# Kernel optimization log

Hardware: AMD Instinct MI355X
Metric: run time of the kernel (lower is better)

The kernel has to match this reference:

```python
import jax, jax.numpy as jnp
import numpy as np

B, L, D, K, NFFT = 4, 8192, 768, 24, 16384


def setup_inputs() -> dict:
    key = jax.random.key(0)
    k1, k2, k3, k4 = jax.random.split(key, 4)
    x = jax.random.normal(k1, (B, L, D), dtype=jnp.float32)
    phi = jax.random.normal(k2, (L, K), dtype=jnp.float32) * 0.1
    M_inputs = jax.random.normal(k3, (D, D), dtype=jnp.float32) * 0.02
    M_filters = jax.random.normal(k4, (K, D), dtype=jnp.float32) * 0.02
    return {"x": x, "phi": phi, "M_inputs": M_inputs, "M_filters": M_filters, "n": NFFT}


def _convolve_approx(u, v, n):
    # u: (B, L, D) projected inputs; v: (L, D) projected filters (per-channel kernels)
    bsz, seq_len, d = u.shape
    sgn = jnp.where(jnp.arange(seq_len) % 2 == 0, 1.0, -1.0).astype(u.dtype)[None, :, None]  # (1,L,1)
    V = jnp.fft.rfft(v.astype(jnp.float32), n=n, axis=0)[None, :, :, None]  # (1,F,D,1)
    U = jnp.stack([u, u * sgn], axis=-1).astype(jnp.float32)  # (B,L,D,2): [plus, sign-flipped]
    Uf = jnp.fft.rfft(U, n=n, axis=1)  # (B,F,D,2)
    conv = jnp.fft.irfft(V * Uf, n=n, axis=1)[:, :seq_len]  # (B,L,D,2)
    U_plus = conv[..., 0]
    U_minus = conv[..., 1] * sgn
    return U_plus, U_minus


def reference(x, phi, M_inputs, M_filters, n):
    x_proj = x @ M_inputs          # (B,L,D)
    phi_proj = phi @ M_filters     # (L,D)
    spectral_plus, spectral_minus = _convolve_approx(x_proj, phi_proj, n)
    return spectral_plus + spectral_minus
```

## Files before the change

### kernel.cpp

```cpp
#include <hip/hip_runtime.h>
#include <stdint.h>

#define B_SZ 4
#define L_SEQ 8192
#define D_CH 768
#define K_F 24
#define NFFT2 8192
#define LDS_BYTES 69632
#define GEMM_LDS 49152

typedef __attribute__((ext_vector_type(4))) float f32x4;
typedef __attribute__((ext_vector_type(8))) __bf16 bf16x8;
typedef __attribute__((ext_vector_type(2))) float v2f;

__device__ __forceinline__ uint32_t f2bf1(float f) {
  uint32_t u = __float_as_uint(f);
  return (u + 0x7fffu + ((u >> 16) & 1u)) >> 16;
}
__device__ __forceinline__ uint32_t packbf2(float lo, float hi) {
  return f2bf1(lo) | (f2bf1(hi) << 16);
}
__device__ __forceinline__ v2f unpackbf2(uint32_t v) {
  return v2f{__uint_as_float(v << 16), __uint_as_float(v & 0xffff0000u)};
}
__device__ __forceinline__ uint32_t pkbf(float lo, float hi) {
  uint32_t r;
  asm("v_cvt_pk_bf16_f32 %0, %1, %2" : "=v"(r) : "v"(lo), "v"(hi));
  return r;
}

__device__ __forceinline__ v2f rotm(v2f v) { return v2f{v.y, -v.x}; }
__device__ __forceinline__ v2f rotp(v2f v) { return v2f{-v.y, v.x}; }
__device__ __forceinline__ v2f cmulf(v2f a, v2f b) {
  return a.x * b + a.y * rotp(b);
}

__device__ __forceinline__ void twfill(v2f* tw) {
  tw[1] = cmulf(tw[0], tw[0]);
  tw[3] = cmulf(tw[1], tw[1]);
  tw[2] = cmulf(tw[0], tw[1]);
  tw[4] = cmulf(tw[3], tw[0]);
  tw[5] = cmulf(tw[3], tw[1]);
  tw[6] = cmulf(tw[3], tw[2]);
}

__global__ __launch_bounds__(256) void k_mit(const float* __restrict__ Mi,
                                             uint16_t* __restrict__ MiT) {
  int i = blockIdx.x * 256 + threadIdx.x;
  int n = i / 768, e = i - n * 768;
  MiT[i] = (uint16_t)f2bf1(Mi[e * 768 + n]);
}

template <int S>
__device__ __forceinline__ void dft8(v2f* x) {
  const float C = 0.70710678118654752f;
  v2f t0 = x[0] + x[4], t1 = x[0] - x[4];
  v2f t2 = x[2] + x[6], t3 = x[2] - x[6];
  v2f t4 = x[1] + x[5], t5 = x[1] - x[5];
  v2f t6 = x[3] + x[7], t7 = x[3] - x[7];
  v2f t3r = (S < 0) ? rotm(t3) : rotp(t3);
  v2f t7r = (S < 0) ? rotm(t7) : rotp(t7);
  v2f e0 = t0 + t2, e2 = t0 - t2;
  v2f e1 = t1 + t3r, e3 = t1 - t3r;
  v2f o0 = t4 + t6, o2 = t4 - t6;
  v2f o1 = t5 + t7r, o3 = t5 - t7r;
  v2f o1r = (S < 0) ? C * (o1 + rotm(o1)) : C * (o1 + rotp(o1));
  v2f o2r = (S < 0) ? rotm(o2) : rotp(o2);
  v2f o3r = (S < 0) ? C * (rotm(o3) - o3) : C * (rotp(o3) - o3);
  x[0] = e0 + o0;
  x[4] = e0 - o0;
  x[1] = e1 + o1r;
  x[5] = e1 - o1r;
  x[2] = e2 + o2r;
  x[6] = e2 - o2r;
  x[3] = e3 + o3r;
  x[7] = e3 - o3r;
}

template <int LH, int S, int NT>
__device__ __forceinline__ void pass_r8(v2f* a, int tid) {
  constexpr int h = 1 << LH;
  constexpr int st = h + (h >> 4);
  const float ang = (S < 0 ? -6.2831853071795864769f : 6.2831853071795864769f) / (float)(h * 8);
  v2f tw[7];
  if constexpr (h <= NT) {
    float sn, cs;
    __sincosf(ang * (float)(tid & (h - 1)), &sn, &cs);
    tw[0] = v2f{cs, sn};
    twfill(tw);
  }
  __syncthreads();
#pragma unroll
  for (int jj = 0; jj < 1024 / NT; ++jj) {
    int j = jj * NT + tid;
    int pos = j & (h - 1);
    int base = ((j >> LH) << (LH + 3)) + pos;
    v2f* p = a + (base + (base >> 4));
    if constexpr (h > NT) {
      float sn, cs;
      __sincosf(ang * (float)pos, &sn, &cs);
      tw[0] = v2f{cs, sn};
      twfill(tw);
    }
    v2f x[8];
#pragma unroll
    for (int q = 0; q < 8; ++q) x[q] = p[q * st];
    if constexpr (S < 0) {
      dft8<-1>(x);
#pragma unroll
      for (int q = 1; q < 8; ++q) x[q] = cmulf(x[q], tw[q - 1]);
    } else {
#pragma unroll
      for (int q = 1; q < 8; ++q) x[q] = cmulf(x[q], tw[q - 1]);
      dft8<1>(x);
    }
#pragma unroll
    for (int q = 0; q < 8; ++q) p[q * st] = x[q];
  }
}

__device__ __forceinline__ void p1_fused(v2f* a, const uint32_t* __restrict__ row32, int tid) {
  const float CP = 0.92387953251128675613f, SP = 0.38268343236508977173f;
  float sn, cs;
  __sincosf(-6.2831853071795864769f / 8192.0f * (float)tid, &sn, &cs);
  v2f w1{cs, sn};
#pragma unroll
  for (int jj = 0; jj < 2; ++jj) {
    int j = jj * 512 + tid;
    v2f x[8];
#pragma unroll
    for (int q = 0; q < 4; ++q) x[q] = unpackbf2(row32[j + q * 1024]);
    x[4] = x[5] = x[6] = x[7] = v2f{0.f, 0.f};
    dft8<-1>(x);
    v2f tw[7];
    tw[0] = w1;
    twfill(tw);
#pragma unroll
    for (int q = 1; q < 8; ++q) x[q] = cmulf(x[q], tw[q - 1]);
    v2f* p = a + (j + (j >> 4));
#pragma unroll
    for (int q = 0; q < 8; ++q) p[q * 1088] = x[q];
    w1 = cmulf(w1, v2f{CP, -SP});
  }
}

__device__ __forceinline__ void mid16(v2f* a, const uint32_t* __restrict__ wrow, int tid) {
  const float C1 = 0.92387953251128675613f, S1 = 0.38268343236508977173f;
  const float C2 = 0.70710678118654752440f;
  __syncthreads();
  int m = tid;
  v2f* p = a + 17 * m;
  v2f e[8], o[8];
#pragma unroll
  for (int q = 0; q < 8; ++q) {
    e[q] = p[2 * q];
    o[q] = p[2 * q + 1];
  }
  dft8<-1>(e);
  dft8<-1>(o);
  o[1] = cmulf(o[1], v2f{C1, -S1});
  o[2] = cmulf(o[2], v2f{C2, -C2});
  o[3] = cmulf(o[3], v2f{S1, -C1});
  o[4] = rotm(o[4]);
  o[5] = cmulf(o[5], v2f{-S1, -C1});
  o[6] = cmulf(o[6], v2f{-C2, -C2});
  o[7] = cmulf(o[7], v2f{-C1, -S1});
  const uint4* wp = (const uint4*)(wrow + 16 * m);
  uint4 w0 = wp[0], w1 = wp[1], w2 = wp[2], w3 = wp[3];
  uint32_t wv[16] = {w0.x, w0.y, w0.z, w0.w, w1.x, w1.y, w1.z, w1.w,
                     w2.x, w2.y, w2.z, w2.w, w3.x, w3.y, w3.z, w3.w};
#pragma unroll
  for (int q = 0; q < 8; ++q) {
    v2f s = e[q] + o[q];
    v2f d = e[q] - o[q];
    s = cmulf(s, unpackbf2(wv[2 * q]));
    d = cmulf(d, unpackbf2(wv[2 * q + 1]));
    e[q] = s + d;
    o[q] = s - d;
  }
  o[1] = cmulf(o[1], v2f{C1, S1});
  o[2] = cmulf(o[2], v2f{C2, C2});
  o[3] = cmulf(o[3], v2f{S1, C1});
  o[4] = rotp(o[4]);
  o[5] = cmulf(o[5], v2f{-S1, C1});
  o[6] = cmulf(o[6], v2f{-C2, C2});
  o[7] = cmulf(o[7], v2f{-C1, S1});
  dft8<1>(e);
  dft8<1>(o);
#pragma unroll
  for (int q = 0; q < 8; ++q) {
    p[2 * q] = e[q];
    p[2 * q + 1] = o[q];
  }
}

__device__ __forceinline__ void last_fused(v2f* a, uint32_t* __restrict__ out32, int tid) {
  const float CP = 0.92387953251128675613f, SP = 0.38268343236508977173f;
  float sn, cs;
  __sincosf(6.2831853071795864769f / 8192.0f * (float)tid, &sn, &cs);
  v2f w1{cs, sn};
  __syncthreads();
#pragma unroll
  for (int jj = 0; jj < 2; ++jj) {
    int j = jj * 512 + tid;
    v2f* p = a + (j + (j >> 4));
    v2f x[8];
#pragma unroll
    for (int q = 0; q < 8; ++q) x[q] = p[q * 1088];
    v2f tw[7];
    tw[0] = w1;
    twfill(tw);
#pragma unroll
    for (int q = 1; q < 8; ++q) x[q] = cmulf(x[q], tw[q - 1]);
    dft8<1>(x);
#pragma unroll
    for (int q = 0; q < 4; ++q) out32[j + q * 1024] = packbf2(x[q].x, x[q].y);
    w1 = cmulf(w1, v2f{CP, SP});
  }
}

__global__ __launch_bounds__(512) void k_phi(const float* __restrict__ phi,
                                             v2f* __restrict__ Phi2) {
  extern __shared__ v2f buf[];
  int k = blockIdx.x, tid = threadIdx.x;
  const float scale = 2.0f / 8192.0f;
  for (int r = tid; r < 4096; r += 512) {
    buf[r + (r >> 4)] = v2f{phi[(2 * r) * K_F + k] * scale, 0.0f};
    int r2i = r + 4096;
    buf[r2i + (r2i >> 4)] = v2f{0.0f, 0.0f};
  }
  pass_r8<10, -1, 512>(buf, tid);
  pass_r8<7, -1, 512>(buf, tid);
  pass_r8<4, -1, 512>(buf, tid);
  pass_r8<1, -1, 512>(buf, tid);
  __syncthreads();
  for (int j = tid; j < 4096; j += 512) {
    v2f* p = buf + (2 * j + ((2 * j) >> 4));
    v2f u = p[0], v = p[1];
    p[0] = u + v;
    p[1] = u - v;
  }
  __syncthreads();
  for (int f = tid; f < NFFT2; f += 512) Phi2[k * NFFT2 + f] = buf[f + (f >> 4)];
}

__global__ __launch_bounds__(256) void k_w2(const v2f* __restrict__ Phi2,
                                            const float* __restrict__ Mf,
                                            uint32_t* __restrict__ W2) {
  __shared__ v2f p[K_F][256];
  __shared__ float mf[K_F][32];
  int tid = threadIdx.x;
  int fc = blockIdx.x & 31, dc = blockIdx.x >> 5;
  int f0 = fc * 256, d0 = dc * 32;
  for (int i = tid; i < K_F * 256; i += 256) {
    int k = i >> 8, fl = i & 255;
    p[k][fl] = Phi2[k * NFFT2 + f0 + fl];
  }
  for (int i = tid; i < K_F * 32; i += 256) {
    int k = i >> 5, dl = i & 31;
    mf[k][dl] = Mf[k * D_CH + d0 + dl];
  }
  __syncthreads();
  for (int dl = 0; dl < 32; ++dl) {
    v2f acc = v2f{0.f, 0.f};
#pragma unroll
    for (int k = 0; k < K_F; ++k) acc += mf[k][dl] * p[k][tid];
    W2[(size_t)(d0 + dl) * NFFT2 + f0 + tid] = packbf2(acc.x, acc.y);
  }
}

__device__ __forceinline__ void gload_lds16(const void* g, void* l) {
  __builtin_amdgcn_global_load_lds(
      (const __attribute__((address_space(1))) void*)g,
      (__attribute__((address_space(3))) void*)l, 16, 0, 0);
}

__global__ __launch_bounds__(256) void k_gemm(const float* __restrict__ X,
                                              const uint16_t* __restrict__ MiT,
                                              uint16_t* __restrict__ Cp) {
  extern __shared__ char lds[];
  char* const As0 = lds;
  char* const Bs0 = lds + 32768;
  int tid = threadIdx.x;
  int lane = tid & 63, wid = tid >> 6;
  int pb = blockIdx.x;
  int v = (pb & 7) * 192 + (pb >> 3);
  int bm = v / 6, bn = v % 6;
  int m0 = bm * 128, n0 = bn * 128;
  int wr = wid >> 1, wc = wid & 1;
  int lm = lane & 15, lg = lane >> 4;
  f32x4 acc[4][4] = {};

#define STAGE_A(k0)                                                     \
  _Pragma("unroll") for (int it = 0; it < 8; ++it) {                    \
    int s = it * 256 + tid;                                             \
    int row = s >> 4, s16 = s & 15;                                     \
    gload_lds16(X + (size_t)(m0 + row) * 768 + (k0) + ((s16 ^ (row & 7)) << 2), \
                As0 + (it * 256 + wid * 64) * 16);                      \
  }
#define STAGE_B(k0)                                                     \
  _Pragma("unroll") for (int it = 0; it < 4; ++it) {                    \
    int s = it * 256 + tid;                                             \
    int row = s >> 3;                                                   \
    int cb = ((s & 7) << 4) ^ ((row & 7) << 4);                         \
    gload_lds16(MiT + (size_t)(n0 + row) * 768 + (k0) + (cb >> 1),      \
                Bs0 + (it * 256 + wid * 64) * 16);                      \
  }

  for (int kt = 0; kt < 12; ++kt) {
    __syncthreads();
    STAGE_A(kt * 64);
    STAGE_B(kt * 64);
    asm volatile("s_waitcnt vmcnt(0)" ::: "memory");
    __syncthreads();
#pragma unroll
    for (int ks = 0; ks < 2; ++ks) {
      bf16x8 a[4], b[4];
#pragma unroll
      for (int mi = 0; mi < 4; ++mi) {
        int row = wr * 64 + mi * 16 + lm;
        const char* rb = As0 + row * 256;
        int s0 = ks * 8 + lg * 2;
        float4 flo = *(const float4*)(rb + ((s0 ^ (row & 7)) << 4));
        float4 fhi = *(const float4*)(rb + (((s0 + 1) ^ (row & 7)) << 4));
        uint4 u;
        u.x = pkbf(flo.x, flo.y);
        u.y = pkbf(flo.z, flo.w);
        u.z = pkbf(fhi.x, fhi.y);
        u.w = pkbf(fhi.z, fhi.w);
        a[mi] = *(const bf16x8*)&u;
      }
      int kbyte = (ks * 32 + lg * 8) * 2;
#pragma unroll
      for (int ni = 0; ni < 4; ++ni) {
        int row = wc * 64 + ni * 16 + lm;
        b[ni] = *(const bf16x8*)(Bs0 + row * 128 + (kbyte ^ ((row & 7) << 4)));
      }
#pragma unroll
      for (int mi = 0; mi < 4; ++mi)
#pragma unroll
        for (int ni = 0; ni < 4; ++ni)
          acc[mi][ni] = __builtin_amdgcn_mfma_f32_16x16x32_bf16(a[mi], b[ni], acc[mi][ni], 0, 0, 0);
    }
  }
#undef STAGE_A
#undef STAGE_B

#pragma unroll
  for (int mi = 0; mi < 4; ++mi) {
#pragma unroll
    for (int ni = 0; ni < 4; ++ni) {
      int mg = m0 + wr * 64 + mi * 16 + lg * 4;
      int dd = n0 + wc * 64 + ni * 16 + lm;
      int bb = mg >> 13, t = mg & 8191;
      f32x4 vv = acc[mi][ni];
      uint2 o;
      o.x = packbf2(vv[0], vv[1]);
      o.y = packbf2(vv[2], vv[3]);
      *(uint2*)(Cp + ((size_t)bb * 768 + dd) * 8192 + t) = o;
    }
  }
}

__global__ __launch_bounds__(512, 4) void k_conv(const uint16_t* __restrict__ xprojT,
                                                 const uint32_t* __restrict__ W2,
                                                 uint16_t* __restrict__ convo) {
  extern __shared__ v2f buf[];
  int tid = threadIdx.x;
  int bd = blockIdx.x;
  int d = bd % 768;
  const uint32_t* row32 = (const uint32_t*)(xprojT + (size_t)bd * 8192);
  p1_fused(buf, row32, tid);
  pass_r8<7, -1, 512>(buf, tid);
  pass_r8<4, -1, 512>(buf, tid);
  mid16(buf, W2 + (size_t)d * NFFT2, tid);
  pass_r8<4, 1, 512>(buf, tid);
  pass_r8<7, 1, 512>(buf, tid);
  last_fused(buf, (uint32_t*)(convo + (size_t)bd * 8192), tid);
}

__global__ __launch_bounds__(256) void k_tr(const uint16_t* __restrict__ convo,
                                            float* __restrict__ out) {
  __shared__ uint16_t tile[64][72];
  int tid = threadIdx.x;
  int bx = blockIdx.x;
  int b = bx / 1536;
  int r = bx - b * 1536;
  int d0 = (r >> 7) << 6;
  int t0 = (r & 127) << 6;
  {
    int rr = tid >> 3;
    int c8 = (tid & 7) << 3;
#pragma unroll
    for (int p = 0; p < 2; ++p) {
      int row = p * 32 + rr;
      uint4 v = *(const uint4*)(convo + ((size_t)(b * 768 + d0 + row)) * 8192 + t0 + c8);
      *(uint4*)&tile[row][c8] = v;
    }
  }
  __syncthreads();
  {
    int c4 = (tid & 15) << 2;
    int tg = tid >> 4;
#pragma unroll
    for (int p = 0; p < 4; ++p) {
      int tt = p * 16 + tg;
      float4 o;
      o.x = __uint_as_float((uint32_t)tile[c4 + 0][tt] << 16);
      o.y = __uint_as_float((uint32_t)tile[c4 + 1][tt] << 16);
      o.z = __uint_as_float((uint32_t)tile[c4 + 2][tt] << 16);
      o.w = __uint_as_float((uint32_t)tile[c4 + 3][tt] << 16);
      *(float4*)(out + ((size_t)b * 8192 + t0 + tt) * 768 + d0 + c4) = o;
    }
  }
}

extern "C" void kernel_launch(void* const* d_in, const int* in_sizes, int n_in,
                              void* d_out, int out_size, void* d_ws, size_t ws_size,
                              hipStream_t stream) {
  const float* x   = (const float*)d_in[0];
  const float* phi = (const float*)d_in[1];
  const float* Mi  = (const float*)d_in[2];
  const float* Mf  = (const float*)d_in[3];
  float* out = (float*)d_out;

  uint16_t* xprojT = (uint16_t*)d_out + 25165824;

  char* ws = (char*)d_ws;
  uint16_t* convo = (uint16_t*)ws;
  uint32_t* W2    = (uint32_t*)(ws + 50331648);
  v2f*      Phi2  = (v2f*)(ws + 75497472);
  uint16_t* MiT   = (uint16_t*)(ws + 77070336);

  k_mit<<<2304, 256, 0, stream>>>(Mi, MiT);
  k_phi<<<24, 512, LDS_BYTES, stream>>>(phi, Phi2);
  k_w2<<<768, 256, 0, stream>>>(Phi2, Mf, W2);
  k_gemm<<<1536, 256, GEMM_LDS, stream>>>(x, MiT, xprojT);
  k_conv<<<3072, 512, LDS_BYTES, stream>>>(xprojT, W2, convo);
  k_tr<<<6144, 256, 0, stream>>>(convo, out);
}
```

Before: 203.1 us.

## Double-buffer GEMM LDS tiles with K-step 32 to overlap loads and MFMA

The input-projection GEMM now prefetches the next K-tile into a second LDS buffer while MFMAs run on the current one. To keep the same LDS footprint, the K tile shrinks from 64 to 32 over 24 iterations, with adjusted swizzles. This hides global-to-LDS load latency behind compute, but it doubles the number of barriers and waitcnts and shortens each compute phase.

```diff
diff --git a/kernel.cpp b/kernel.cpp
--- a/kernel.cpp
+++ b/kernel.cpp
@@ -291,57 +291,59 @@
   int lm = lane & 15, lg = lane >> 4;
   f32x4 acc[4][4] = {};
 
-#define STAGE_A(k0)                                                     \
-  _Pragma("unroll") for (int it = 0; it < 8; ++it) {                    \
-    int s = it * 256 + tid;                                             \
-    int row = s >> 4, s16 = s & 15;                                     \
-    gload_lds16(X + (size_t)(m0 + row) * 768 + (k0) + ((s16 ^ (row & 7)) << 2), \
-                As0 + (it * 256 + wid * 64) * 16);                      \
-  }
-#define STAGE_B(k0)                                                     \
+#define STAGE_A(bufc, k0)                                               \
   _Pragma("unroll") for (int it = 0; it < 4; ++it) {                    \
     int s = it * 256 + tid;                                             \
-    int row = s >> 3;                                                   \
-    int cb = ((s & 7) << 4) ^ ((row & 7) << 4);                         \
-    gload_lds16(MiT + (size_t)(n0 + row) * 768 + (k0) + (cb >> 1),      \
-                Bs0 + (it * 256 + wid * 64) * 16);                      \
-  }
-
-  for (int kt = 0; kt < 12; ++kt) {
-    __syncthreads();
-    STAGE_A(kt * 64);
-    STAGE_B(kt * 64);
+    int row = s >> 3, s8 = s & 7;                                       \
+    gload_lds16(X + (size_t)(m0 + row) * 768 + (k0) + ((s8 ^ (row & 7)) << 2), \
+                As0 + (bufc) * 16384 + (it * 256 + wid * 64) * 16);     \
+  }
+#define STAGE_B(bufc, k0)                                               \
+  _Pragma("unroll") for (int it = 0; it < 2; ++it) {                    \
+    int s = it * 256 + tid;                                             \
+    int row = s >> 2, s4 = s & 3;                                       \
+    gload_lds16(MiT + (size_t)(n0 + row) * 768 + (k0) + ((s4 ^ (row & 3)) << 3), \
+                Bs0 + (bufc) * 8192 + (it * 256 + wid * 64) * 16);      \
+  }
+
+  STAGE_A(0, 0);
+  STAGE_B(0, 0);
+  asm volatile("s_waitcnt vmcnt(0)" ::: "memory");
+  __syncthreads();
+
+#pragma unroll
+  for (int kt = 0; kt < 24; ++kt) {
+    const int cur = kt & 1;
+    if (kt < 23) {
+      STAGE_A(cur ^ 1, (kt + 1) * 32);
+      STAGE_B(cur ^ 1, (kt + 1) * 32);
+    }
+    bf16x8 a[4], b[4];
+#pragma unroll
+    for (int mi = 0; mi < 4; ++mi) {
+      int row = wr * 64 + mi * 16 + lm;
+      const char* rb = As0 + cur * 16384 + row * 128;
+      float4 flo = *(const float4*)(rb + (((2 * lg) ^ (row & 7)) << 4));
+      float4 fhi = *(const float4*)(rb + (((2 * lg + 1) ^ (row & 7)) << 4));
+      uint4 u;
+      u.x = pkbf(flo.x, flo.y);
+      u.y = pkbf(flo.z, flo.w);
+      u.z = pkbf(fhi.x, fhi.y);
+      u.w = pkbf(fhi.z, fhi.w);
+      a[mi] = *(const bf16x8*)&u;
+    }
+#pragma unroll
+    for (int ni = 0; ni < 4; ++ni) {
+      int row = wc * 64 + ni * 16 + lm;
+      b[ni] = *(const bf16x8*)(Bs0 + cur * 8192 + row * 64 + ((lg ^ (row & 3)) << 4));
+    }
+#pragma unroll
+    for (int mi = 0; mi < 4; ++mi)
+#pragma unroll
+      for (int ni = 0; ni < 4; ++ni)
+        acc[mi][ni] = __builtin_amdgcn_mfma_f32_16x16x32_bf16(a[mi], b[ni], acc[mi][ni], 0, 0, 0);
     asm volatile("s_waitcnt vmcnt(0)" ::: "memory");
     __syncthreads();
-#pragma unroll
-    for (int ks = 0; ks < 2; ++ks) {
-      bf16x8 a[4], b[4];
-#pragma unroll
-      for (int mi = 0; mi < 4; ++mi) {
-        int row = wr * 64 + mi * 16 + lm;
-        const char* rb = As0 + row * 256;
-        int s0 = ks * 8 + lg * 2;
-        float4 flo = *(const float4*)(rb + ((s0 ^ (row & 7)) << 4));
-        float4 fhi = *(const float4*)(rb + (((s0 + 1) ^ (row & 7)) << 4));
-        uint4 u;
-        u.x = pkbf(flo.x, flo.y);
-        u.y = pkbf(flo.z, flo.w);
-        u.z = pkbf(fhi.x, fhi.y);
-        u.w = pkbf(fhi.z, fhi.w);
-        a[mi] = *(const bf16x8*)&u;
-      }
-      int kbyte = (ks * 32 + lg * 8) * 2;
-#pragma unroll
-      for (int ni = 0; ni < 4; ++ni) {
-        int row = wc * 64 + ni * 16 + lm;
-        b[ni] = *(const bf16x8*)(Bs0 + row * 128 + (kbyte ^ ((row & 7) << 4)));
-      }
-#pragma unroll
-      for (int mi = 0; mi < 4; ++mi)
-#pragma unroll
-        for (int ni = 0; ni < 4; ++ni)
-          acc[mi][ni] = __builtin_amdgcn_mfma_f32_16x16x32_bf16(a[mi], b[ni], acc[mi][ni], 0, 0, 0);
-    }
   }
 #undef STAGE_A
 #undef STAGE_B
```

Result: slower. 208.6 us (+2.7%).
